# Kernel tuning notes

Hardware: AMD Instinct MI355X
Metric: run time of the kernel (lower is better)

Reference implementation:

```python
import jax, jax.numpy as jnp
import numpy as np

B, L, N, D, H, DFF, LAYERS, PRED = 16, 96, 512, 512, 8, 2048, 2, 96
NMARK = 4
WINDOWS = (4, 8, 12, 24)
EPS_REVIN = 1e-5


def layernorm(x, g, b, eps=1e-5):
    m = x.mean(-1, keepdims=True)
    v = ((x - m) ** 2).mean(-1, keepdims=True)
    return (x - m) * jax.lax.rsqrt(v + eps) * g + b


def moving_avg(x, w):
    # replicate-pad left by w-1, then window-mean of size w (stride 1) -> same length
    p = jnp.pad(x, ((0, 0), (w - 1, 0), (0, 0)), mode='edge')
    c = jnp.cumsum(p, axis=1)
    c = jnp.concatenate([jnp.zeros_like(c[:, :1]), c], axis=1)
    return (c[:, w:] - c[:, :-w]) / w


def trend_guidance(x, w1, b1, w2, b2):
    # x: [B, L, N]
    trend_stack = jnp.stack([moving_avg(x, w) for w in WINDOWS], axis=-1)  # [B,L,N,W]
    mean_f = x.mean(axis=1)
    std_f = jnp.sqrt(x.var(axis=1) + 1e-6)
    stats = jnp.stack([mean_f, std_f], axis=-1)  # [B,N,2]
    h = jax.nn.relu(stats @ w1 + b1)
    weights = jax.nn.softmax(h @ w2 + b2, axis=-1)  # [B,N,W]
    trend = (trend_stack * weights[:, None]).sum(-1)  # [B,L,N]
    tf = trend.transpose(0, 2, 1)  # [B,N,L]
    nt = tf / jnp.maximum(jnp.linalg.norm(tf, axis=-1, keepdims=True), 1e-12)
    return nt @ nt.transpose(0, 2, 1)  # [B,N,N]


def enc_layer(x, guide_full, wq, bq, wk, bk, wv, bv, wo, bo, w1, b1, w2, b2, l1g, l1b, l2g, l2b):
    Bq, T, Dm = x.shape
    E = Dm // H
    q = (x @ wq + bq).reshape(Bq, T, H, E)
    k = (x @ wk + bk).reshape(Bq, T, H, E)
    v = (x @ wv + bv).reshape(Bq, T, H, E)
    scores = jnp.einsum('blhe,bshe->bhls', q, k) / jnp.sqrt(jnp.asarray(E, x.dtype))
    attn = jax.nn.softmax(scores, axis=-1)
    attn = attn * guide_full[:, None]                      # sigmoid guidance gate
    attn = attn / (attn.sum(-1, keepdims=True) + 1e-6)     # renormalize
    ctx = jnp.einsum('bhls,bshd->blhd', attn, v).reshape(Bq, T, Dm)
    x = x + (ctx @ wo + bo)
    x = layernorm(x, l1g, l1b)
    y = jax.nn.gelu(x @ w1 + b1, approximate=False)
    y = y @ w2 + b2
    return layernorm(x + y, l2g, l2b)


def setup_inputs():
    key = jax.random.key(0)
    ks = iter(jax.random.split(key, 64))
    def nrm(shape, s=0.02):
        return jax.random.normal(next(ks), shape, jnp.float32) * s
    return {
        'x_enc': jax.random.normal(next(ks), (B, L, N), jnp.float32),
        'x_mark_enc': jax.random.normal(next(ks), (B, L, NMARK), jnp.float32),
        'x_dec': jnp.zeros((1, 1, 1), jnp.float32),
        'x_mark_dec': jnp.zeros((1, 1, 1), jnp.float32),
        'gamma': jnp.ones((1, 1, N), jnp.float32),
        'beta': jnp.zeros((1, 1, N), jnp.float32),
        'tp_w1': nrm((2, 16), 0.5), 'tp_b1': jnp.zeros((16,), jnp.float32),
        'tp_w2': nrm((16, len(WINDOWS)), 0.5), 'tp_b2': jnp.zeros((len(WINDOWS),), jnp.float32),
        'emb_w': nrm((L, D)), 'emb_b': jnp.zeros((D,), jnp.float32),
        'wq': nrm((LAYERS, D, D)), 'bq': jnp.zeros((LAYERS, D), jnp.float32),
        'wk': nrm((LAYERS, D, D)), 'bk': jnp.zeros((LAYERS, D), jnp.float32),
        'wv': nrm((LAYERS, D, D)), 'bv': jnp.zeros((LAYERS, D), jnp.float32),
        'wo': nrm((LAYERS, D, D)), 'bo': jnp.zeros((LAYERS, D), jnp.float32),
        'w1': nrm((LAYERS, D, DFF)), 'b1': jnp.zeros((LAYERS, DFF), jnp.float32),
        'w2': nrm((LAYERS, DFF, D)), 'b2': jnp.zeros((LAYERS, D), jnp.float32),
        'ln1g': jnp.ones((LAYERS, D), jnp.float32), 'ln1b': jnp.zeros((LAYERS, D), jnp.float32),
        'ln2g': jnp.ones((LAYERS, D), jnp.float32), 'ln2b': jnp.zeros((LAYERS, D), jnp.float32),
        'normg': jnp.ones((D,), jnp.float32), 'normb': jnp.zeros((D,), jnp.float32),
        'proj_w': nrm((D, PRED)), 'proj_b': jnp.zeros((PRED,), jnp.float32),
    }


def reference(x_enc, x_mark_enc, x_dec, x_mark_dec, gamma, beta, tp_w1, tp_b1, tp_w2, tp_b2,
              emb_w, emb_b, wq, bq, wk, bk, wv, bv, wo, bo, w1, b1, w2, b2,
              ln1g, ln1b, ln2g, ln2b, normg, normb, proj_w, proj_b):
    Bq, Lq, Nq = x_enc.shape
    # RevIN
    mean = x_enc.mean(1, keepdims=True)
    std = jnp.sqrt(x_enc.var(1, keepdims=True) + EPS_REVIN)
    x_norm = (x_enc - mean) / std * gamma + beta
    # trend guidance [B,N,N]
    guidance = trend_guidance(x_norm, tp_w1, tp_b1, tp_w2, tp_b2)
    # inverted embedding: variates + time-mark features as tokens
    tok = jnp.concatenate([x_norm.transpose(0, 2, 1), x_mark_enc.transpose(0, 2, 1)], axis=1)  # [B,T,L]
    x = tok @ emb_w + emb_b  # [B,T,D]
    T = x.shape[1]
    guide_full = jnp.full((Bq, T, T), 0.5, x.dtype).at[:, :Nq, :Nq].set(jax.nn.sigmoid(guidance))
    for i in range(LAYERS):
        x = enc_layer(x, guide_full, wq[i], bq[i], wk[i], bk[i], wv[i], bv[i], wo[i], bo[i],
                      w1[i], b1[i], w2[i], b2[i], ln1g[i], ln1b[i], ln2g[i], ln2b[i])
    x = layernorm(x, normg, normb)
    dec = (x @ proj_w + proj_b).transpose(0, 2, 1)[:, :, :Nq]  # [B,pred_len,N]
    dec = (dec - beta) / (gamma + EPS_REVIN) * std + mean       # RevIN inverse
    return dec[:, -PRED:, :]
```

## Files before the change

kernel.cpp:

```cpp
#include <hip/hip_runtime.h>
#include <hip/hip_bf16.h>
#include <math.h>

#define B 16
#define L 96
#define N 512
#define D 512
#define H 8
#define E 64
#define DFF 2048
#define T 516
#define PRED 96
#define NMARK 4
#define VTS 576
#define NCHUNK 9

typedef __attribute__((ext_vector_type(8))) short bf16x8;
typedef __attribute__((ext_vector_type(4))) float f32x4;

#define WS_MEAN 0
#define WS_STD  32768
#define WS_GD   65536
#define WS_X    8454144
#define WS_XB   25362432
#define WS_WTS  33816576
#define WS_QB   46596096
#define WS_KB   55050240
#define WS_VT   63504384
#define VT_BYTES 9437184

#define WT_WQ   0u
#define WT_WK   524288u
#define WT_WV   1048576u
#define WT_WO   1572864u
#define WT_W1   2097152u
#define WT_W2   4194304u
#define WT_EMB  6291456u
#define WT_PROJ 6340608u

__global__ void revin_stats_kernel(const float* __restrict__ x, float* __restrict__ mean,
                                   float* __restrict__ stdv) {
    int i = blockIdx.x * blockDim.x + threadIdx.x;
    if (i >= B * N) return;
    int b = i >> 9;
    int n = i & (N - 1);
    const float* p = x + (size_t)b * L * N + n;
    float s = 0.f, ss = 0.f;
    for (int l = 0; l < L; ++l) {
        float v = p[(size_t)l * N];
        s += v; ss += v * v;
    }
    float m = s / (float)L;
    float var = ss / (float)L - m * m;
    mean[i] = m;
    stdv[i] = sqrtf(fmaxf(var, 0.f) + 1e-5f);
}

__global__ void norm_transpose_kernel(const float* __restrict__ x, const float* __restrict__ mean,
                                      const float* __restrict__ stdv, const float* __restrict__ gamma,
                                      const float* __restrict__ beta, float* __restrict__ xt) {
    int idx = blockIdx.x * blockDim.x + threadIdx.x;
    if (idx >= B * N * L) return;
    int l = idx % L;
    int n = (idx / L) % N;
    int b = idx / (L * N);
    float v = x[((size_t)b * L + l) * N + n];
    int bn = b * N + n;
    xt[idx] = (v - mean[bn]) / stdv[bn] * gamma[n] + beta[n];
}

__global__ void trend_nt_kernel(const float* __restrict__ xt, const float* __restrict__ tp_w1,
                                const float* __restrict__ tp_b1, const float* __restrict__ tp_w2,
                                const float* __restrict__ tp_b2, float* __restrict__ nt) {
    int bn = blockIdx.x;
    __shared__ float xr[96];
    __shared__ float P[97];
    __shared__ float wt[4];
    __shared__ float tr[96];
    __shared__ float nrm;
    int tid = threadIdx.x;
    if (tid < 96) xr[tid] = xt[(size_t)bn * 96 + tid];
    __syncthreads();
    if (tid == 0) {
        float s = 0.f, ss = 0.f;
        P[0] = 0.f;
        for (int l = 0; l < 96; ++l) { s += xr[l]; P[l + 1] = s; ss += xr[l] * xr[l]; }
        float m = s / 96.f;
        float var = ss / 96.f - m * m;
        float sd = sqrtf(fmaxf(var, 0.f) + 1e-6f);
        float h[16];
        for (int j = 0; j < 16; ++j) {
            float t = m * tp_w1[j] + sd * tp_w1[16 + j] + tp_b1[j];
            h[j] = fmaxf(t, 0.f);
        }
        float lg[4];
        for (int w = 0; w < 4; ++w) {
            float t = tp_b2[w];
            for (int j = 0; j < 16; ++j) t += h[j] * tp_w2[j * 4 + w];
            lg[w] = t;
        }
        float mx = fmaxf(fmaxf(lg[0], lg[1]), fmaxf(lg[2], lg[3]));
        float es = 0.f;
        for (int w = 0; w < 4; ++w) { lg[w] = expf(lg[w] - mx); es += lg[w]; }
        for (int w = 0; w < 4; ++w) wt[w] = lg[w] / es;
    }
    __syncthreads();
    const int WS[4] = {4, 8, 12, 24};
    if (tid < 96) {
        int l = tid;
        float t = 0.f;
        for (int wi = 0; wi < 4; ++wi) {
            int w = WS[wi];
            int lo = l - w + 1;
            float s;
            if (lo >= 0) s = P[l + 1] - P[lo];
            else         s = P[l + 1] - P[0] + (float)(-lo) * xr[0];
            t += (s / (float)w) * wt[wi];
        }
        tr[l] = t;
    }
    __syncthreads();
    if (tid == 0) {
        float s = 0.f;
        for (int l = 0; l < 96; ++l) s += tr[l] * tr[l];
        nrm = fmaxf(sqrtf(s), 1e-12f);
    }
    __syncthreads();
    if (tid < 96) nt[(size_t)bn * 96 + tid] = tr[tid] / nrm;
}

__global__ void guide_kernel(const float* __restrict__ nt, __hip_bfloat16* __restrict__ guide) {
    __shared__ float ri[16][97];
    __shared__ float rj[16][97];
    int b = blockIdx.z;
    int i0 = blockIdx.y * 16;
    int j0 = blockIdx.x * 16;
    int tx = threadIdx.x, ty = threadIdx.y;
    int tid = ty * 16 + tx;
    for (int t = tid; t < 16 * 96; t += 256) {
        int r = t / 96, c = t % 96;
        ri[r][c] = nt[((size_t)b * N + i0 + r) * 96 + c];
        rj[r][c] = nt[((size_t)b * N + j0 + r) * 96 + c];
    }
    __syncthreads();
    float acc = 0.f;
    for (int k = 0; k < 96; ++k) acc += ri[ty][k] * rj[tx][k];
    guide[((size_t)b * N + i0 + ty) * N + j0 + tx] =
        __float2bfloat16(1.f / (1.f + expf(-acc)));
}

__global__ void build_tok_kernel(const float* __restrict__ xt, const float* __restrict__ xmark,
                                 __hip_bfloat16* __restrict__ tok) {
    int idx = blockIdx.x * blockDim.x + threadIdx.x;
    if (idx >= B * T * L) return;
    int l = idx % L;
    int t = (idx / L) % T;
    int b = idx / (L * T);
    float v;
    if (t < N) v = xt[((size_t)b * N + t) * L + l];
    else       v = xmark[((size_t)b * L + l) * NMARK + (t - N)];
    tok[idx] = __float2bfloat16(v);
}

__global__ void wconv_kernel(const float* __restrict__ wq, const float* __restrict__ wk,
                             const float* __restrict__ wv, const float* __restrict__ wo,
                             const float* __restrict__ w1, const float* __restrict__ w2,
                             const float* __restrict__ emb, const float* __restrict__ proj,
                             __hip_bfloat16* __restrict__ wts) {
    int bid = blockIdx.x;
    const float* src; __hip_bfloat16* dst; int K, Nn, tloc;
    if (bid < 2048) {
        int seg = bid >> 9;
        int t = bid & 511;
        int layer = t >> 8;
        tloc = t & 255;
        K = 512; Nn = 512;
        const float* bases[4] = {wq, wk, wv, wo};
        src = bases[seg] + (size_t)layer * 512 * 512;
        dst = wts + (seg == 0 ? WT_WQ : seg == 1 ? WT_WK : seg == 2 ? WT_WV : WT_WO)
                  + (size_t)layer * 512 * 512;
    } else if (bid < 4096) {
        int t = bid - 2048;
        int layer = t >> 10;
        tloc = t & 1023;
        K = 512; Nn = 2048;
        src = w1 + (size_t)layer * 512 * 2048;
        dst = wts + WT_W1 + (size_t)layer * 2048 * 512;
    } else if (bid < 6144) {
        int t = bid - 4096;
        int layer = t >> 10;
        tloc = t & 1023;
        K = 2048; Nn = 512;
        src = w2 + (size_t)layer * 2048 * 512;
        dst = wts + WT_W2 + (size_t)layer * 512 * 2048;
    } else if (bid < 6192) {
        tloc = bid - 6144;
        K = 96; Nn = 512;
        src = emb; dst = wts + WT_EMB;
    } else {
        tloc = bid - 6192;
        K = 512; Nn = 96;
        src = proj; dst = wts + WT_PROJ;
    }
    int ntile = Nn >> 5;
    int tk = tloc / ntile, tn = tloc % ntile;
    int k0 = tk * 32, n0 = tn * 32;
    __shared__ float ld[32][33];
    int tid = threadIdx.x;
    for (int i = tid; i < 1024; i += 256) {
        int r = i >> 5, c = i & 31;
        ld[r][c] = src[(size_t)(k0 + r) * Nn + n0 + c];
    }
    __syncthreads();
    for (int i = tid; i < 1024; i += 256) {
        int r = i >> 5, c = i & 31;
        dst[(size_t)(n0 + r) * K + k0 + c] = __float2bfloat16(ld[c][r]);
    }
}

template<int TM, int TN>
__global__ __launch_bounds__(256, 2) void mfma_gemm_t(
    const __hip_bfloat16* __restrict__ A, const __hip_bfloat16* __restrict__ Wt,
    const float* __restrict__ bias, const float* __restrict__ res,
    float* __restrict__ outF, __hip_bfloat16* __restrict__ outB,
    int M, int Nn, int K, int act, int vtmode, int nbm, int nbn) {
    constexpr int WM = TM / 2, WN = TN / 2;
    constexpr int FI = WM / 16, FJ = WN / 16;
    __shared__ __align__(16) __hip_bfloat16 As[TM * 32];
    __shared__ __align__(16) __hip_bfloat16 Bs[TN * 32];
    int id = blockIdx.x;
    int xcd = id & 7, slot = id >> 3;
    int bmb = xcd + 8 * (slot / nbn);
    int bnb = slot % nbn;
    if (bmb >= nbm) return;
    int bm = bmb * TM;
    int bn = bnb * TN;
    int tid = threadIdx.x;
    int lane = tid & 63;
    int wave = tid >> 6;
    int col = lane & 15;
    int quad = lane >> 4;
    int wm = (wave & 1) * WM;
    int wn = (wave >> 1) * WN;
    f32x4 acc[FI][FJ];
    #pragma unroll
    for (int i = 0; i < FI; ++i)
        #pragma unroll
        for (int j = 0; j < FJ; ++j) acc[i][j] = (f32x4){0.f, 0.f, 0.f, 0.f};

    for (int k0 = 0; k0 < K; k0 += 32) {
        #pragma unroll
        for (int cc = 0; cc < TM / 64; ++cc) {
            int cbase = cc * 256 + wave * 64;
            int c = cbase + lane;
            int gm = bm + (c >> 2); if (gm >= M) gm = M - 1;
            const __hip_bfloat16* ga = A + (size_t)gm * K + k0 + (c & 3) * 8;
            __builtin_amdgcn_global_load_lds(
                (const __attribute__((address_space(1))) void*)ga,
                (__attribute__((address_space(3))) void*)(As + (size_t)cbase * 8), 16, 0, 0);
        }
        #pragma unroll
        for (int cc = 0; cc < TN / 64; ++cc) {
            int cbase = cc * 256 + wave * 64;
            int c = cbase + lane;
            int gn = bn + (c >> 2); if (gn >= Nn) gn = Nn - 1;
            const __hip_bfloat16* gb = Wt + (size_t)gn * K + k0 + (c & 3) * 8;
            __builtin_amdgcn_global_load_lds(
                (const __attribute__((address_space(1))) void*)gb,
                (__attribute__((address_space(3))) void*)(Bs + (size_t)cbase * 8), 16, 0, 0);
        }
        __syncthreads();
        bf16x8 af[FI], bfr[FJ];
        #pragma unroll
        for (int i = 0; i < FI; ++i)
            af[i] = *(const bf16x8*)(const void*)&As[(wm + i * 16 + col) * 32 + quad * 8];
        #pragma unroll
        for (int j = 0; j < FJ; ++j)
            bfr[j] = *(const bf16x8*)(const void*)&Bs[(wn + j * 16 + col) * 32 + quad * 8];
        #pragma unroll
        for (int i = 0; i < FI; ++i)
            #pragma unroll
            for (int j = 0; j < FJ; ++j)
                acc[i][j] = __builtin_amdgcn_mfma_f32_16x16x32_bf16(af[i], bfr[j], acc[i][j], 0, 0, 0);
        __syncthreads();
    }
    #pragma unroll
    for (int i = 0; i < FI; ++i) {
        int gmb = bm + wm + i * 16 + quad * 4;
        #pragma unroll
        for (int j = 0; j < FJ; ++j) {
            int gn = bn + wn + j * 16 + col;
            if (gn >= Nn) continue;
            float bs = bias[gn];
            #pragma unroll
            for (int r = 0; r < 4; ++r) {
                int gm = gmb + r;
                if (gm >= M) continue;
                float v = acc[i][j][r] + bs;
                if (act == 1) v = 0.5f * v * (1.f + erff(v * 0.70710678118654752f));
                if (res) v += res[(size_t)gm * Nn + gn];
                if (outF) outF[(size_t)gm * Nn + gn] = v;
                if (outB) {
                    if (vtmode) {
                        int bb = gm / T;
                        int tt = gm - bb * T;
                        outB[((size_t)bb * 512 + gn) * VTS + tt] = __float2bfloat16(v);
                    } else {
                        outB[(size_t)gm * Nn + gn] = __float2bfloat16(v);
                    }
                }
            }
        }
    }
}

__global__ __launch_bounds__(256) void attn_flash_kernel(
    const __hip_bfloat16* __restrict__ qb, const __hip_bfloat16* __restrict__ kb,
    const __hip_bfloat16* __restrict__ vt, const __hip_bfloat16* __restrict__ gd,
    __hip_bfloat16* __restrict__ ctxb) {
    __shared__ __align__(16) __hip_bfloat16 Ks[64][72];
    __shared__ __align__(16) __hip_bfloat16 Vs[64][72];
    __shared__ __align__(16) __hip_bfloat16 Pw[4][16][72];
    __shared__ __align__(16) __hip_bfloat16 Gs[64][68];
    int bid = blockIdx.x;
    int sg = bid % 9;
    int h = (bid / 9) % H;
    int b = bid / (9 * H);
    int tid = threadIdx.x;
    int wave = tid >> 6, lane = tid & 63;
    int col = lane & 15, quad = lane >> 4;
    int q0b = sg * 64;
    int q0 = q0b + wave * 16;

    int qr = q0 + col; if (qr > T - 1) qr = T - 1;
    const __hip_bfloat16* qptr = qb + (size_t)(b * T + qr) * D + h * E + quad * 8;
    bf16x8 a0 = *(const bf16x8*)(const void*)qptr;
    bf16x8 a1 = *(const bf16x8*)(const void*)(qptr + 32);

    float m_r[4] = {-1e30f, -1e30f, -1e30f, -1e30f};
    float S[4] = {0.f, 0.f, 0.f, 0.f};
    float G[4] = {0.f, 0.f, 0.f, 0.f};
    f32x4 o[4];
    #pragma unroll
    for (int j = 0; j < 4; ++j) o[j] = (f32x4){0.f, 0.f, 0.f, 0.f};

    const __hip_bfloat16* vbase = vt + (size_t)((b * H + h) * E) * VTS;

    for (int kc = 0; kc < NCHUNK; ++kc) {
        __syncthreads();
        #pragma unroll
        for (int i = 0; i < 2; ++i) {
            int idx = tid + i * 256;
            int r = idx >> 3, s = idx & 7;
            int kr = kc * 64 + r; int krc = kr > T - 1 ? T - 1 : kr;
            *(bf16x8*)(void*)&Ks[r][s * 8] =
                *(const bf16x8*)(const void*)(kb + (size_t)(b * T + krc) * D + h * E + s * 8);
            *(bf16x8*)(void*)&Vs[r][s * 8] =
                *(const bf16x8*)(const void*)(vbase + (size_t)r * VTS + kc * 64 + s * 8);
            bf16x8 gval;
            int grow = q0b + r;
            if (grow < N && kc < 8) {
                gval = *(const bf16x8*)(const void*)(gd + ((size_t)b * N + grow) * N + kc * 64 + s * 8);
            } else {
                gval = (bf16x8){0x3F00, 0x3F00, 0x3F00, 0x3F00, 0x3F00, 0x3F00, 0x3F00, 0x3F00};
            }
            *(bf16x8*)(void*)&Gs[r][s * 8] = gval;
        }
        __syncthreads();
        f32x4 sc[4];
        #pragma unroll
        for (int sub = 0; sub < 4; ++sub) {
            bf16x8 b0 = *(const bf16x8*)(const void*)&Ks[sub * 16 + col][quad * 8];
            bf16x8 b1 = *(const bf16x8*)(const void*)&Ks[sub * 16 + col][32 + quad * 8];
            f32x4 acc = (f32x4){0.f, 0.f, 0.f, 0.f};
            acc = __builtin_amdgcn_mfma_f32_16x16x32_bf16(a0, b0, acc, 0, 0, 0);
            acc = __builtin_amdgcn_mfma_f32_16x16x32_bf16(a1, b1, acc, 0, 0, 0);
            sc[sub] = acc;
        }
        float cm[4] = {-1e30f, -1e30f, -1e30f, -1e30f};
        #pragma unroll
        for (int sub = 0; sub < 4; ++sub) {
            int key = kc * 64 + sub * 16 + col;
            #pragma unroll
            for (int r = 0; r < 4; ++r) {
                float v = sc[sub][r] * 0.125f;
                if (key >= T) v = -1e30f;
                sc[sub][r] = v;
                cm[r] = fmaxf(cm[r], v);
            }
        }
        #pragma unroll
        for (int r = 0; r < 4; ++r)
            #pragma unroll
            for (int d = 1; d < 16; d <<= 1) cm[r] = fmaxf(cm[r], __shfl_xor(cm[r], d, 64));
        float alpha[4];
        #pragma unroll
        for (int r = 0; r < 4; ++r) {
            float mn = fmaxf(m_r[r], cm[r]);
            alpha[r] = __expf(m_r[r] - mn);
            m_r[r] = mn;
            S[r] *= alpha[r];
            G[r] *= alpha[r];
        }
        #pragma unroll
        for (int j = 0; j < 4; ++j)
            #pragma unroll
            for (int r = 0; r < 4; ++r) o[j][r] *= alpha[r];
        #pragma unroll
        for (int sub = 0; sub < 4; ++sub) {
            #pragma unroll
            for (int r = 0; r < 4; ++r) {
                float p = __expf(sc[sub][r] - m_r[r]);
                S[r] += p;
                float g = __bfloat162float(Gs[wave * 16 + quad * 4 + r][sub * 16 + col]);
                float t = p * g;
                G[r] += t;
                Pw[wave][quad * 4 + r][sub * 16 + col] = __float2bfloat16(t);
            }
        }
        #pragma unroll
        for (int ks = 0; ks < 2; ++ks) {
            bf16x8 pa = *(const bf16x8*)(const void*)&Pw[wave][col][ks * 32 + quad * 8];
            #pragma unroll
            for (int j = 0; j < 4; ++j) {
                bf16x8 bv = *(const bf16x8*)(const void*)&Vs[j * 16 + col][ks * 32 + quad * 8];
                o[j] = __builtin_amdgcn_mfma_f32_16x16x32_bf16(pa, bv, o[j], 0, 0, 0);
            }
        }
    }
    #pragma unroll
    for (int r = 0; r < 4; ++r) {
        #pragma unroll
        for (int d = 1; d < 16; d <<= 1) {
            S[r] += __shfl_xor(S[r], d, 64);
            G[r] += __shfl_xor(G[r], d, 64);
        }
    }
    float inv[4];
    #pragma unroll
    for (int r = 0; r < 4; ++r) inv[r] = 1.f / (G[r] + 1e-6f * S[r]);
    #pragma unroll
    for (int j = 0; j < 4; ++j)
        #pragma unroll
        for (int r = 0; r < 4; ++r) {
            int row = q0 + quad * 4 + r;
            if (row < T)
                ctxb[(size_t)(b * T + row) * D + h * E + j * 16 + col] =
                    __float2bfloat16(o[j][r] * inv[r]);
        }
}

__global__ __launch_bounds__(256) void ln_kernel(const float* __restrict__ in, const float* __restrict__ g,
                          const float* __restrict__ bb, float* __restrict__ outF,
                          __hip_bfloat16* __restrict__ outB) {
    int row = blockIdx.x * 4 + (threadIdx.x >> 6);
    int lane = threadIdx.x & 63;
    const float* base = in + (size_t)row * D + lane * 8;
    float4 u0 = *(const float4*)base;
    float4 u1 = *(const float4*)(base + 4);
    float s = (u0.x + u0.y) + (u0.z + u0.w) + (u1.x + u1.y) + (u1.z + u1.w);
    float ss = u0.x * u0.x + u0.y * u0.y + u0.z * u0.z + u0.w * u0.w
             + u1.x * u1.x + u1.y * u1.y + u1.z * u1.z + u1.w * u1.w;
    #pragma unroll
    for (int d = 1; d < 64; d <<= 1) {
        s += __shfl_xor(s, d, 64);
        ss += __shfl_xor(ss, d, 64);
    }
    float m = s * (1.f / (float)D);
    float var = ss * (1.f / (float)D) - m * m;
    float rstd = rsqrtf(fmaxf(var, 0.f) + 1e-5f);
    float4 g0 = *(const float4*)(g + lane * 8);
    float4 g1 = *(const float4*)(g + lane * 8 + 4);
    float4 b0 = *(const float4*)(bb + lane * 8);
    float4 b1 = *(const float4*)(bb + lane * 8 + 4);
    float4 o0, o1;
    o0.x = (u0.x - m) * rstd * g0.x + b0.x;
    o0.y = (u0.y - m) * rstd * g0.y + b0.y;
    o0.z = (u0.z - m) * rstd * g0.z + b0.z;
    o0.w = (u0.w - m) * rstd * g0.w + b0.w;
    o1.x = (u1.x - m) * rstd * g1.x + b1.x;
    o1.y = (u1.y - m) * rstd * g1.y + b1.y;
    o1.z = (u1.z - m) * rstd * g1.z + b1.z;
    o1.w = (u1.w - m) * rstd * g1.w + b1.w;
    *(float4*)(outF + (size_t)row * D + lane * 8) = o0;
    *(float4*)(outF + (size_t)row * D + lane * 8 + 4) = o1;
    __align__(16) __hip_bfloat16 tmp[8];
    tmp[0] = __float2bfloat16(o0.x); tmp[1] = __float2bfloat16(o0.y);
    tmp[2] = __float2bfloat16(o0.z); tmp[3] = __float2bfloat16(o0.w);
    tmp[4] = __float2bfloat16(o1.x); tmp[5] = __float2bfloat16(o1.y);
    tmp[6] = __float2bfloat16(o1.z); tmp[7] = __float2bfloat16(o1.w);
    *(bf16x8*)(void*)(outB + (size_t)row * D + lane * 8) = *(const bf16x8*)(const void*)tmp;
}

__global__ __launch_bounds__(256) void revin_inv_kernel(
    const float* __restrict__ dec, const float* __restrict__ beta,
    const float* __restrict__ gamma, const float* __restrict__ mean,
    const float* __restrict__ stdv, float* __restrict__ out) {
    __shared__ float tile[64][33];
    int b = blockIdx.x;
    int n0 = blockIdx.y * 64;
    int p0 = blockIdx.z * 32;
    int t = threadIdx.x;
    int pl = t & 31, nb = t >> 5;
    #pragma unroll
    for (int i = 0; i < 8; ++i) {
        int nl = nb + i * 8;
        tile[nl][pl] = dec[((size_t)b * T + n0 + nl) * PRED + p0 + pl];
    }
    __syncthreads();
    int nl = t & 63, pb = t >> 6;
    int n = n0 + nl;
    int bn = b * N + n;
    float be = beta[n], ga = gamma[n], sd = stdv[bn], mn = mean[bn];
    float scale = sd / (ga + 1e-5f);
    #pragma unroll
    for (int i = 0; i < 8; ++i) {
        int p = p0 + pb + i * 4;
        out[((size_t)b * PRED + p) * N + n] = (tile[nl][pb + i * 4] - be) * scale + mn;
    }
}

static inline int swz_grid(int nbm, int nbn) { return 8 * ((nbm + 7) / 8) * nbn; }

extern "C" void kernel_launch(void* const* d_in, const int* in_sizes, int n_in,
                              void* d_out, int out_size, void* d_ws, size_t ws_size,
                              hipStream_t stream) {
    const float* x_enc  = (const float*)d_in[0];
    const float* x_mark = (const float*)d_in[1];
    const float* gamma  = (const float*)d_in[4];
    const float* beta   = (const float*)d_in[5];
    const float* tp_w1  = (const float*)d_in[6];
    const float* tp_b1  = (const float*)d_in[7];
    const float* tp_w2  = (const float*)d_in[8];
    const float* tp_b2  = (const float*)d_in[9];
    const float* emb_w  = (const float*)d_in[10];
    const float* emb_b  = (const float*)d_in[11];
    const float* wq = (const float*)d_in[12];
    const float* bq = (const float*)d_in[13];
    const float* wk = (const float*)d_in[14];
    const float* bk = (const float*)d_in[15];
    const float* wv = (const float*)d_in[16];
    const float* bv = (const float*)d_in[17];
    const float* wo = (const float*)d_in[18];
    const float* bo = (const float*)d_in[19];
    const float* w1 = (const float*)d_in[20];
    const float* b1 = (const float*)d_in[21];
    const float* w2 = (const float*)d_in[22];
    const float* b2 = (const float*)d_in[23];
    const float* ln1g = (const float*)d_in[24];
    const float* ln1b = (const float*)d_in[25];
    const float* ln2g = (const float*)d_in[26];
    const float* ln2b = (const float*)d_in[27];
    const float* normg = (const float*)d_in[28];
    const float* normb = (const float*)d_in[29];
    const float* proj_w = (const float*)d_in[30];
    const float* proj_b = (const float*)d_in[31];

    char* ws = (char*)d_ws;
    float* mean = (float*)(ws + WS_MEAN);
    float* stdv = (float*)(ws + WS_STD);
    __hip_bfloat16* gd  = (__hip_bfloat16*)(ws + WS_GD);
    float* x            = (float*)(ws + WS_X);
    __hip_bfloat16* xb  = (__hip_bfloat16*)(ws + WS_XB);
    __hip_bfloat16* wts = (__hip_bfloat16*)(ws + WS_WTS);
    __hip_bfloat16* qbuf = (__hip_bfloat16*)(ws + WS_QB);
    __hip_bfloat16* kbuf = (__hip_bfloat16*)(ws + WS_KB);
    __hip_bfloat16* vt   = (__hip_bfloat16*)(ws + WS_VT);
    float* xt  = (float*)(ws + WS_KB);
    float* nt  = (float*)(ws + WS_VT);
    __hip_bfloat16* tokb = (__hip_bfloat16*)(ws + WS_QB);
    __hip_bfloat16* ctxb = xb;
    __hip_bfloat16* ffnb = (__hip_bfloat16*)(ws + WS_QB);
    float* dec = (float*)(ws + WS_QB);

    revin_stats_kernel<<<(B * N + 255) / 256, 256, 0, stream>>>(x_enc, mean, stdv);
    norm_transpose_kernel<<<(B * N * L + 255) / 256, 256, 0, stream>>>(x_enc, mean, stdv, gamma, beta, xt);
    trend_nt_kernel<<<B * N, 128, 0, stream>>>(xt, tp_w1, tp_b1, tp_w2, tp_b2, nt);
    guide_kernel<<<dim3(N / 16, N / 16, B), dim3(16, 16), 0, stream>>>(nt, gd);
    hipMemsetAsync(vt, 0, VT_BYTES, stream);
    build_tok_kernel<<<(B * T * L + 255) / 256, 256, 0, stream>>>(xt, x_mark, tokb);
    wconv_kernel<<<6240, 256, 0, stream>>>(wq, wk, wv, wo, w1, w2, emb_w, proj_w, wts);

    const int M = B * T;
    const int NBM64 = (M + 63) / 64;
    const int NBM128 = (M + 127) / 128;
    mfma_gemm_t<64, 64><<<swz_grid(NBM64, 8), 256, 0, stream>>>(
        tokb, wts + WT_EMB, emb_b, nullptr, x, xb, M, D, L, 0, 0, NBM64, 8);
    for (int i = 0; i < 2; ++i) {
        const __hip_bfloat16* wqT = wts + WT_WQ + (size_t)i * D * D;
        const __hip_bfloat16* wkT = wts + WT_WK + (size_t)i * D * D;
        const __hip_bfloat16* wvT = wts + WT_WV + (size_t)i * D * D;
        const __hip_bfloat16* woT = wts + WT_WO + (size_t)i * D * D;
        mfma_gemm_t<64, 64><<<swz_grid(NBM64, 8), 256, 0, stream>>>(
            xb, wqT, bq + i * D, nullptr, nullptr, qbuf, M, D, D, 0, 0, NBM64, 8);
        mfma_gemm_t<64, 64><<<swz_grid(NBM64, 8), 256, 0, stream>>>(
            xb, wkT, bk + i * D, nullptr, nullptr, kbuf, M, D, D, 0, 0, NBM64, 8);
        mfma_gemm_t<64, 64><<<swz_grid(NBM64, 8), 256, 0, stream>>>(
            xb, wvT, bv + i * D, nullptr, nullptr, vt, M, D, D, 0, 1, NBM64, 8);
        attn_flash_kernel<<<B * H * 9, 256, 0, stream>>>(qbuf, kbuf, vt, gd, ctxb);
        mfma_gemm_t<64, 64><<<swz_grid(NBM64, 8), 256, 0, stream>>>(
            ctxb, woT, bo + i * D, x, x, nullptr, M, D, D, 0, 0, NBM64, 8);
        ln_kernel<<<M / 4, 256, 0, stream>>>(x, ln1g + i * D, ln1b + i * D, x, xb);
        mfma_gemm_t<128, 128><<<swz_grid(NBM128, 16), 256, 0, stream>>>(
            xb, wts + WT_W1 + (size_t)i * DFF * D, b1 + i * DFF, nullptr,
            nullptr, ffnb, M, DFF, D, 1, 0, NBM128, 16);
        mfma_gemm_t<64, 64><<<swz_grid(NBM64, 8), 256, 0, stream>>>(
            ffnb, wts + WT_W2 + (size_t)i * DFF * D, b2 + i * D, x, x, nullptr,
            M, D, DFF, 0, 0, NBM64, 8);
        ln_kernel<<<M / 4, 256, 0, stream>>>(x, ln2g + i * D, ln2b + i * D, x, xb);
    }
    ln_kernel<<<M / 4, 256, 0, stream>>>(x, normg, normb, x, xb);
    mfma_gemm_t<64, 64><<<swz_grid(NBM64, 2), 256, 0, stream>>>(
        xb, wts + WT_PROJ, proj_b, nullptr, dec, nullptr, M, PRED, D, 0, 0, NBM64, 2);
    revin_inv_kernel<<<dim3(B, N / 64, PRED / 32), 256, 0, stream>>>(dec, beta, gamma, mean, stdv,
                                                                     (float*)d_out);
}
```

Before: 730.3 us.

## Fuse Q/K/V projections into one GEMM and XOR-swizzle GEMM LDS tiles

Packs the transposed Q, K and V weights contiguously per layer and replaces the three separate projection launches with a single qkv_gemm whose epilogue routes each column block to q, k or the transposed v buffer. This cuts launch count and gives one larger grid with better occupancy. Separately, all MFMA GEMMs now XOR-swizzle the 16-byte segments within each LDS row, on both the global-to-LDS load and the fragment reads, to reduce LDS bank conflicts. The swizzle has to stay consistent between the load and read paths, and the fused kernel adds branching in its epilogue.

New measurement: 722.9 us. No clear change (-1.0%).

```diff
diff --git a/kernel.cpp b/kernel.cpp
--- a/kernel.cpp
+++ b/kernel.cpp
@@ -29,9 +29,7 @@
 #define WS_VT   63504384
 #define VT_BYTES 9437184
 
-#define WT_WQ   0u
-#define WT_WK   524288u
-#define WT_WV   1048576u
+#define WT_QKV  0u
 #define WT_WO   1572864u
 #define WT_W1   2097152u
 #define WT_W2   4194304u
@@ -177,8 +175,10 @@
         K = 512; Nn = 512;
         const float* bases[4] = {wq, wk, wv, wo};
         src = bases[seg] + (size_t)layer * 512 * 512;
-        dst = wts + (seg == 0 ? WT_WQ : seg == 1 ? WT_WK : seg == 2 ? WT_WV : WT_WO)
-                  + (size_t)layer * 512 * 512;
+        if (seg < 3)
+            dst = wts + WT_QKV + (size_t)layer * 1536 * 512 + (size_t)seg * 512 * 512;
+        else
+            dst = wts + WT_WO + (size_t)layer * 512 * 512;
     } else if (bid < 4096) {
         int t = bid - 2048;
         int layer = t >> 10;
@@ -217,6 +217,9 @@
         dst[(size_t)(n0 + r) * K + k0 + c] = __float2bfloat16(ld[c][r]);
     }
 }
+
+#define SWZ_SEG(c, row) (((c) & 3) ^ (((row) >> 1) & 3))
+#define SWZ_RD(row, quad) (((row) * 4 + ((quad) ^ (((row) >> 1) & 3))) * 8)
 
 template<int TM, int TN>
 __global__ __launch_bounds__(256, 2) void mfma_gemm_t(
@@ -253,8 +256,10 @@
         for (int cc = 0; cc < TM / 64; ++cc) {
             int cbase = cc * 256 + wave * 64;
             int c = cbase + lane;
-            int gm = bm + (c >> 2); if (gm >= M) gm = M - 1;
-            const __hip_bfloat16* ga = A + (size_t)gm * K + k0 + (c & 3) * 8;
+            int row = c >> 2;
+            int seg = SWZ_SEG(c, row);
+            int gm = bm + row; if (gm >= M) gm = M - 1;
+            const __hip_bfloat16* ga = A + (size_t)gm * K + k0 + seg * 8;
             __builtin_amdgcn_global_load_lds(
                 (const __attribute__((address_space(1))) void*)ga,
                 (__attribute__((address_space(3))) void*)(As + (size_t)cbase * 8), 16, 0, 0);
@@ -263,8 +268,10 @@
         for (int cc = 0; cc < TN / 64; ++cc) {
             int cbase = cc * 256 + wave * 64;
             int c = cbase + lane;
-            int gn = bn + (c >> 2); if (gn >= Nn) gn = Nn - 1;
-            const __hip_bfloat16* gb = Wt + (size_t)gn * K + k0 + (c & 3) * 8;
+            int row = c >> 2;
+            int seg = SWZ_SEG(c, row);
+            int gn = bn + row; if (gn >= Nn) gn = Nn - 1;
+            const __hip_bfloat16* gb = Wt + (size_t)gn * K + k0 + seg * 8;
             __builtin_amdgcn_global_load_lds(
                 (const __attribute__((address_space(1))) void*)gb,
                 (__attribute__((address_space(3))) void*)(Bs + (size_t)cbase * 8), 16, 0, 0);
@@ -272,11 +279,15 @@
         __syncthreads();
         bf16x8 af[FI], bfr[FJ];
         #pragma unroll
-        for (int i = 0; i < FI; ++i)
-            af[i] = *(const bf16x8*)(const void*)&As[(wm + i * 16 + col) * 32 + quad * 8];
-        #pragma unroll
-        for (int j = 0; j < FJ; ++j)
-            bfr[j] = *(const bf16x8*)(const void*)&Bs[(wn + j * 16 + col) * 32 + quad * 8];
+        for (int i = 0; i < FI; ++i) {
+            int ra = wm + i * 16 + col;
+            af[i] = *(const bf16x8*)(const void*)&As[SWZ_RD(ra, quad)];
+        }
+        #pragma unroll
+        for (int j = 0; j < FJ; ++j) {
+            int rb = wn + j * 16 + col;
+            bfr[j] = *(const bf16x8*)(const void*)&Bs[SWZ_RD(rb, quad)];
+        }
         #pragma unroll
         for (int i = 0; i < FI; ++i)
             #pragma unroll
@@ -308,6 +319,97 @@
                     } else {
                         outB[(size_t)gm * Nn + gn] = __float2bfloat16(v);
                     }
+                }
+            }
+        }
+    }
+}
+
+__global__ __launch_bounds__(256, 2) void qkv_gemm(
+    const __hip_bfloat16* __restrict__ A, const __hip_bfloat16* __restrict__ Wt,
+    const float* __restrict__ bq, const float* __restrict__ bk, const float* __restrict__ bv,
+    __hip_bfloat16* __restrict__ qb, __hip_bfloat16* __restrict__ kb,
+    __hip_bfloat16* __restrict__ vt, int nbm, int nbn) {
+    const int M = B * T, K = D, Nn = 1536;
+    __shared__ __align__(16) __hip_bfloat16 As[64 * 32];
+    __shared__ __align__(16) __hip_bfloat16 Bs[64 * 32];
+    int id = blockIdx.x;
+    int xcd = id & 7, slot = id >> 3;
+    int bmb = xcd + 8 * (slot / nbn);
+    int bnb = slot % nbn;
+    if (bmb >= nbm) return;
+    int bm = bmb * 64;
+    int bn = bnb * 64;
+    int tid = threadIdx.x;
+    int lane = tid & 63;
+    int wave = tid >> 6;
+    int col = lane & 15;
+    int quad = lane >> 4;
+    int wm = (wave & 1) * 32;
+    int wn = (wave >> 1) * 32;
+    f32x4 acc[2][2];
+    #pragma unroll
+    for (int i = 0; i < 2; ++i)
+        #pragma unroll
+        for (int j = 0; j < 2; ++j) acc[i][j] = (f32x4){0.f, 0.f, 0.f, 0.f};
+
+    for (int k0 = 0; k0 < K; k0 += 32) {
+        {
+            int cbase = wave * 64;
+            int c = cbase + lane;
+            int row = c >> 2;
+            int seg = SWZ_SEG(c, row);
+            int gm = bm + row; if (gm >= M) gm = M - 1;
+            const __hip_bfloat16* ga = A + (size_t)gm * K + k0 + seg * 8;
+            __builtin_amdgcn_global_load_lds(
+                (const __attribute__((address_space(1))) void*)ga,
+                (__attribute__((address_space(3))) void*)(As + (size_t)cbase * 8), 16, 0, 0);
+            int gn = bn + row;
+            const __hip_bfloat16* gb = Wt + (size_t)gn * K + k0 + seg * 8;
+            __builtin_amdgcn_global_load_lds(
+                (const __attribute__((address_space(1))) void*)gb,
+                (__attribute__((address_space(3))) void*)(Bs + (size_t)cbase * 8), 16, 0, 0);
+        }
+        __syncthreads();
+        bf16x8 af[2], bfr[2];
+        #pragma unroll
+        for (int i = 0; i < 2; ++i) {
+            int ra = wm + i * 16 + col;
+            af[i] = *(const bf16x8*)(const void*)&As[SWZ_RD(ra, quad)];
+        }
+        #pragma unroll
+        for (int j = 0; j < 2; ++j) {
+            int rb = wn + j * 16 + col;
+            bfr[j] = *(const bf16x8*)(const void*)&Bs[SWZ_RD(rb, quad)];
+        }
+        #pragma unroll
+        for (int i = 0; i < 2; ++i)
+            #pragma unroll
+            for (int j = 0; j < 2; ++j)
+                acc[i][j] = __builtin_amdgcn_mfma_f32_16x16x32_bf16(af[i], bfr[j], acc[i][j], 0, 0, 0);
+        __syncthreads();
+    }
+    int sel = bn >> 9;
+    const float* bias = sel == 0 ? bq : sel == 1 ? bk : bv;
+    #pragma unroll
+    for (int i = 0; i < 2; ++i) {
+        int gmb = bm + wm + i * 16 + quad * 4;
+        #pragma unroll
+        for (int j = 0; j < 2; ++j) {
+            int gn = bn + wn + j * 16 + col;
+            int gl = gn & 511;
+            float bs = bias[gl];
+            #pragma unroll
+            for (int r = 0; r < 4; ++r) {
+                int gm = gmb + r;
+                if (gm >= M) continue;
+                float v = acc[i][j][r] + bs;
+                if (sel == 0)      qb[(size_t)gm * 512 + gl] = __float2bfloat16(v);
+                else if (sel == 1) kb[(size_t)gm * 512 + gl] = __float2bfloat16(v);
+                else {
+                    int bb = gm / T;
+                    int tt = gm - bb * T;
+                    vt[((size_t)bb * 512 + gl) * VTS + tt] = __float2bfloat16(v);
                 }
             }
         }
@@ -587,16 +689,10 @@
     mfma_gemm_t<64, 64><<<swz_grid(NBM64, 8), 256, 0, stream>>>(
         tokb, wts + WT_EMB, emb_b, nullptr, x, xb, M, D, L, 0, 0, NBM64, 8);
     for (int i = 0; i < 2; ++i) {
-        const __hip_bfloat16* wqT = wts + WT_WQ + (size_t)i * D * D;
-        const __hip_bfloat16* wkT = wts + WT_WK + (size_t)i * D * D;
-        const __hip_bfloat16* wvT = wts + WT_WV + (size_t)i * D * D;
-        const __hip_bfloat16* woT = wts + WT_WO + (size_t)i * D * D;
-        mfma_gemm_t<64, 64><<<swz_grid(NBM64, 8), 256, 0, stream>>>(
-            xb, wqT, bq + i * D, nullptr, nullptr, qbuf, M, D, D, 0, 0, NBM64, 8);
-        mfma_gemm_t<64, 64><<<swz_grid(NBM64, 8), 256, 0, stream>>>(
-            xb, wkT, bk + i * D, nullptr, nullptr, kbuf, M, D, D, 0, 0, NBM64, 8);
-        mfma_gemm_t<64, 64><<<swz_grid(NBM64, 8), 256, 0, stream>>>(
-            xb, wvT, bv + i * D, nullptr, nullptr, vt, M, D, D, 0, 1, NBM64, 8);
+        const __hip_bfloat16* qkvT = wts + WT_QKV + (size_t)i * 1536 * 512;
+        const __hip_bfloat16* woT  = wts + WT_WO + (size_t)i * D * D;
+        qkv_gemm<<<swz_grid(NBM64, 24), 256, 0, stream>>>(
+            xb, qkvT, bq + i * D, bk + i * D, bv + i * D, qbuf, kbuf, vt, NBM64, 24);
         attn_flash_kernel<<<B * H * 9, 256, 0, stream>>>(qbuf, kbuf, vt, gd, ctxb);
         mfma_gemm_t<64, 64><<<swz_grid(NBM64, 8), 256, 0, stream>>>(
             ctxb, woT, bo + i * D, x, x, nullptr, M, D, D, 0, 0, NBM64, 8);
```
